# Kernel tuning notes

Measured on AMD Instinct MI355X. Metric: run time of the kernel, lower is better.

## Reference

```python
import jax, jax.numpy as jnp
import numpy as np

D_MODEL = 2048
HIDDEN = 1024
NUM_EXPERTS = 8
TOTAL_TOKENS = 16384  # tokens already sorted/grouped by expert


def setup_inputs() -> dict:
    key = jax.random.key(0)
    k1, k2, k3 = jax.random.split(key, 3)
    x = jax.random.normal(k1, (TOTAL_TOKENS, D_MODEL), dtype=jnp.float32)
    # nn.Linear(d_model, 2*E*H).weight -> [2*E*H, d_model]
    w_up_gate = jax.random.normal(k2, (2 * NUM_EXPERTS * HIDDEN, D_MODEL), dtype=jnp.float32) / np.sqrt(D_MODEL)
    # nn.Linear(E*H, d_model).weight -> [d_model, E*H]
    w_down = jax.random.normal(k3, (D_MODEL, NUM_EXPERTS * HIDDEN), dtype=jnp.float32) / np.sqrt(HIDDEN)
    batch_size_per_expert = jnp.full((NUM_EXPERTS,), TOTAL_TOKENS // NUM_EXPERTS, dtype=jnp.int32)
    return {
        "x": x,
        "w_up_gate": w_up_gate,
        "w_down": w_down,
        "batch_size_per_expert": batch_size_per_expert,
        "num_experts": NUM_EXPERTS,
    }


def reference(x, w_up_gate, w_down, batch_size_per_expert, num_experts):
    # Per-expert sizes are host constants (a Python list in the torch code).
    sizes = np.asarray(batch_size_per_expert)
    offs = np.concatenate([[0], np.cumsum(sizes)])  # static token offsets
    d_model = x.shape[-1]
    hidden = w_up_gate.shape[0] // (2 * num_experts)
    # [E, 2H, d_model]: expert e's fused up/gate weight block
    w_ug = w_up_gate.reshape(num_experts, 2 * hidden, d_model)
    outs = []
    for e in range(num_experts):  # small static loop over experts (ragged grouped GEMM)
        xe = x[offs[e]:offs[e + 1]]                      # [n_e, d_model]
        ug = xe @ w_ug[e].T                              # [n_e, 2H]
        h = jax.nn.silu(ug[:, :hidden]) * ug[:, hidden:]  # SwiGLU, [n_e, H]
        wd_e = w_down[:, e * hidden:(e + 1) * hidden]    # [d_model, H]
        outs.append(h @ wd_e.T)                          # [n_e, d_model]
    return jnp.concatenate(outs, axis=0)
```

## Files before the change

### kernel.cpp

```cpp
#include <hip/hip_runtime.h>
#include <hip/hip_bf16.h>

typedef __attribute__((ext_vector_type(8))) short short8;
typedef __attribute__((ext_vector_type(4))) float float4v;

#define BM 128
#define BK 32
#define LDSK 40

struct alignas(8) BF4 { unsigned short x, y, z, w; };
struct alignas(16) I4 { int x, y, z, w; };

__device__ __forceinline__ unsigned short f2bf(float f) {
    union { float f; unsigned u; } v; v.f = f;
    unsigned u = v.u + (0x7FFFu + ((v.u >> 16) & 1u));
    return (unsigned short)(u >> 16);
}

__device__ __forceinline__ void stage_f32_tile(const float* __restrict__ src, long ld,
                                               unsigned short* lds, int t) {
    const int rr  = t >> 3;
    const int col = (t & 7) << 2;
    #pragma unroll
    for (int r = 0; r < 4; ++r) {
        const int row = rr + r * 32;
        const float4 v = *(const float4*)(src + (long)row * ld + col);
        BF4 o; o.x = f2bf(v.x); o.y = f2bf(v.y); o.z = f2bf(v.z); o.w = f2bf(v.w);
        *(BF4*)(lds + row * LDSK + col) = o;
    }
}

__device__ __forceinline__ int find_expert(const int* __restrict__ bspe, int row0) {
    int e = 0, off = 0;
    #pragma unroll
    for (int i = 0; i < 8; ++i) {
        int s = bspe[i];
        if (row0 < off + s) { e = i; break; }
        off += s;
    }
    return e;
}

__global__ __launch_bounds__(256) void moe_up_gate(
    const float* __restrict__ x, const float* __restrict__ wug,
    const int* __restrict__ bspe, unsigned short* __restrict__ hws) {
    __shared__ alignas(16) unsigned short As[BM * LDSK];
    __shared__ alignas(16) unsigned short Bs[BM * LDSK];

    const int t = threadIdx.x;
    const int lane = t & 63;
    const int w = t >> 6;
    const int wr = w >> 1, wc = w & 1;
    const int bm = blockIdx.y;
    const int h0 = blockIdx.x * 64;
    const int row0 = bm * BM;

    const int e = find_expert(bspe, row0);

    const float* abase = x + (long)row0 * 2048;
    const float* bup = wug + ((long)e * 2048 + h0) * 2048;
    const float* bgt = wug + ((long)e * 2048 + 1024 + h0) * 2048;

    float4v acc[4][4];
    #pragma unroll
    for (int m = 0; m < 4; ++m)
        #pragma unroll
        for (int n = 0; n < 4; ++n)
            acc[m][n] = (float4v){0.f, 0.f, 0.f, 0.f};

    const int k8 = (lane >> 4) << 3;
    const int am = wr * 64 + (lane & 15);
    const int l15 = lane & 15;

    for (int k0 = 0; k0 < 2048; k0 += BK) {
        __syncthreads();
        stage_f32_tile(abase + k0, 2048, As, t);
        {
            const int rr  = t >> 3;
            const int col = (t & 7) << 2;
            #pragma unroll
            for (int r = 0; r < 4; ++r) {
                const int row = rr + r * 32;
                const float* p = (row < 64 ? bup + (long)row * 2048
                                           : bgt + (long)(row - 64) * 2048) + k0 + col;
                const float4 v = *(const float4*)p;
                BF4 o; o.x = f2bf(v.x); o.y = f2bf(v.y); o.z = f2bf(v.z); o.w = f2bf(v.w);
                *(BF4*)(Bs + row * LDSK + col) = o;
            }
        }
        __syncthreads();

        short8 a[4], b[4];
        #pragma unroll
        for (int m = 0; m < 4; ++m)
            a[m] = *(const short8*)(As + (am + m * 16) * LDSK + k8);
        #pragma unroll
        for (int n = 0; n < 4; ++n) {
            const int rb = (n < 2) ? (wc * 32 + n * 16) : (64 + wc * 32 + (n - 2) * 16);
            b[n] = *(const short8*)(Bs + (rb + l15) * LDSK + k8);
        }
        #pragma unroll
        for (int m = 0; m < 4; ++m)
            #pragma unroll
            for (int n = 0; n < 4; ++n)
                acc[m][n] = __builtin_amdgcn_mfma_f32_16x16x32_bf16(a[m], b[n], acc[m][n], 0, 0, 0);
    }

    const int rbase = row0 + wr * 64 + (lane >> 4) * 4;
    const int cbase = h0 + wc * 32 + l15;
    #pragma unroll
    for (int m = 0; m < 4; ++m)
        #pragma unroll
        for (int n = 0; n < 2; ++n)
            #pragma unroll
            for (int q = 0; q < 4; ++q) {
                const float u = acc[m][n][q];
                const float g = acc[m][n + 2][q];
                const float s = u / (1.f + __expf(-u));
                const int row = rbase + m * 16 + q;
                const int col = cbase + n * 16;
                hws[(long)row * 1024 + col] = f2bf(s * g);
            }
}

__global__ __launch_bounds__(256) void moe_down(
    const unsigned short* __restrict__ hws, const float* __restrict__ wd,
    const int* __restrict__ bspe, float* __restrict__ out) {
    __shared__ alignas(16) unsigned short As[BM * LDSK];
    __shared__ alignas(16) unsigned short Bs[BM * LDSK];

    const int t = threadIdx.x;
    const int lane = t & 63;
    const int w = t >> 6;
    const int wr = w >> 1, wc = w & 1;
    const int bm = blockIdx.y;
    const int n0 = blockIdx.x * BM;
    const int row0 = bm * BM;

    const int e = find_expert(bspe, row0);

    const unsigned short* abase = hws + (long)row0 * 1024;
    const float* bbase = wd + (long)n0 * 8192 + e * 1024;

    float4v acc[4][4];
    #pragma unroll
    for (int m = 0; m < 4; ++m)
        #pragma unroll
        for (int n = 0; n < 4; ++n)
            acc[m][n] = (float4v){0.f, 0.f, 0.f, 0.f};

    const int k8 = (lane >> 4) << 3;
    const int am = wr * 64 + (lane & 15);
    const int l15 = lane & 15;

    for (int k0 = 0; k0 < 1024; k0 += BK) {
        __syncthreads();
        {
            const int row = t >> 2;
            const int col = (t & 3) << 3;
            #pragma unroll
            for (int r = 0; r < 2; ++r) {
                const I4 v = *(const I4*)(abase + (long)(row + r * 64) * 1024 + k0 + col);
                *(I4*)(As + (row + r * 64) * LDSK + col) = v;
            }
        }
        stage_f32_tile(bbase + k0, 8192, Bs, t);
        __syncthreads();

        short8 a[4], b[4];
        #pragma unroll
        for (int m = 0; m < 4; ++m)
            a[m] = *(const short8*)(As + (am + m * 16) * LDSK + k8);
        #pragma unroll
        for (int n = 0; n < 4; ++n)
            b[n] = *(const short8*)(Bs + (wc * 64 + n * 16 + l15) * LDSK + k8);
        #pragma unroll
        for (int m = 0; m < 4; ++m)
            #pragma unroll
            for (int n = 0; n < 4; ++n)
                acc[m][n] = __builtin_amdgcn_mfma_f32_16x16x32_bf16(a[m], b[n], acc[m][n], 0, 0, 0);
    }

    const int rbase = row0 + wr * 64 + (lane >> 4) * 4;
    const int cbase = n0 + wc * 64 + l15;
    #pragma unroll
    for (int m = 0; m < 4; ++m)
        #pragma unroll
        for (int n = 0; n < 4; ++n)
            #pragma unroll
            for (int q = 0; q < 4; ++q)
                out[(long)(rbase + m * 16 + q) * 2048 + cbase + n * 16] = acc[m][n][q];
}

extern "C" void kernel_launch(void* const* d_in, const int* in_sizes, int n_in,
                              void* d_out, int out_size, void* d_ws, size_t ws_size,
                              hipStream_t stream) {
    const float* x   = (const float*)d_in[0];
    const float* wug = (const float*)d_in[1];
    const float* wd  = (const float*)d_in[2];
    const int*  bspe = (const int*)d_in[3];
    float* out = (float*)d_out;
    unsigned short* hws = (unsigned short*)d_ws;

    moe_up_gate<<<dim3(16, 128), dim3(256), 0, stream>>>(x, wug, bspe, hws);
    moe_down  <<<dim3(16, 128), dim3(256), 0, stream>>>(hws, wd, bspe, out);
}
```

Measured before the change: 680.8 us.

## Pre-convert inputs to bf16 and stage GEMM tiles via async global-to-LDS loads

Adds a single conversion kernel that casts x, the up/gate weights and the down weights to bf16 in workspace. Both grouped GEMMs then read bf16 directly and copy tiles into LDS with global_load_lds, replacing the per-tile fp32 load and convert in every block. This removes redundant re-conversion of the same tiles across blocks and halves the bytes read in the GEMM loops. In exchange it adds an extra pass over about 84M floats, needs a large workspace (otherwise the old fp32 path runs), and drops the LDS row padding, which may cause bank conflicts.

```diff
diff --git a/kernel.cpp b/kernel.cpp
--- a/kernel.cpp
+++ b/kernel.cpp
@@ -9,6 +9,7 @@
 #define LDSK 40
 
 struct alignas(8) BF4 { unsigned short x, y, z, w; };
+struct alignas(16) BF8 { BF4 a, b; };
 struct alignas(16) I4 { int x, y, z, w; };
 
 __device__ __forceinline__ unsigned short f2bf(float f) {
@@ -17,9 +18,188 @@
     return (unsigned short)(u >> 16);
 }
 
+__device__ __forceinline__ void async_copy16(const unsigned short* g, unsigned short* l) {
+    __builtin_amdgcn_global_load_lds(
+        (const __attribute__((address_space(1))) void*)g,
+        (__attribute__((address_space(3))) void*)l, 16, 0, 0);
+}
+
+__device__ __forceinline__ int find_expert(const int* __restrict__ bspe, int row0) {
+    int e = 0, off = 0;
+    #pragma unroll
+    for (int i = 0; i < 8; ++i) {
+        int s = bspe[i];
+        if (row0 < off + s) { e = i; break; }
+        off += s;
+    }
+    return e;
+}
+
+#define NX  33554432L
+#define NUG 33554432L
+#define NWD 16777216L
+
+__global__ void cvt_all(const float* __restrict__ x, const float* __restrict__ wug,
+                        const float* __restrict__ wd,
+                        unsigned short* __restrict__ xbf, unsigned short* __restrict__ wugbf,
+                        unsigned short* __restrict__ wdbf) {
+    const long TOT8 = (NX + NUG + NWD) / 8;
+    for (long i = (long)blockIdx.x * blockDim.x + threadIdx.x; i < TOT8;
+         i += (long)gridDim.x * blockDim.x) {
+        const long e0 = i * 8;
+        const float* s; unsigned short* d;
+        if (e0 < NX)            { s = x   + e0;              d = xbf   + e0; }
+        else if (e0 < NX + NUG) { s = wug + (e0 - NX);       d = wugbf + (e0 - NX); }
+        else                    { s = wd  + (e0 - NX - NUG); d = wdbf  + (e0 - NX - NUG); }
+        const float4 a = *(const float4*)s;
+        const float4 b = *(const float4*)(s + 4);
+        BF8 o;
+        o.a.x = f2bf(a.x); o.a.y = f2bf(a.y); o.a.z = f2bf(a.z); o.a.w = f2bf(a.w);
+        o.b.x = f2bf(b.x); o.b.y = f2bf(b.y); o.b.z = f2bf(b.z); o.b.w = f2bf(b.w);
+        *(BF8*)d = o;
+    }
+}
+
+__global__ __launch_bounds__(256) void moe_up_gate_v2(
+    const unsigned short* __restrict__ xbf, const unsigned short* __restrict__ wugbf,
+    const int* __restrict__ bspe, unsigned short* __restrict__ hbf) {
+    __shared__ alignas(16) unsigned short As[BM * BK];
+    __shared__ alignas(16) unsigned short Bs[BM * BK];
+
+    const int t = threadIdx.x, lane = t & 63, w = t >> 6;
+    const int wr = w >> 1, wc = w & 1;
+    const int h0 = blockIdx.x * 64, row0 = blockIdx.y * BM;
+    const int e = find_expert(bspe, row0);
+
+    const int srow = lane >> 2;
+    const int scol = (lane & 3) * 8;
+    const long aoff0 = (long)(row0 + w * 16 + srow) * 2048 + scol;
+    const long aoff1 = aoff0 + 64L * 2048;
+    const int brow = w * 16 + srow;
+    const long boff_up = ((long)e * 2048 + h0 + brow) * 2048 + scol;
+    const long boff_gt = ((long)e * 2048 + 1024 + h0 + brow) * 2048 + scol;
+    unsigned short* lA0 = As + w * 512;
+    unsigned short* lA1 = As + 2048 + w * 512;
+    unsigned short* lB0 = Bs + w * 512;
+    unsigned short* lB1 = Bs + 2048 + w * 512;
+
+    float4v acc[4][4];
+    #pragma unroll
+    for (int m = 0; m < 4; ++m)
+        #pragma unroll
+        for (int n = 0; n < 4; ++n) acc[m][n] = (float4v){0.f, 0.f, 0.f, 0.f};
+
+    const int k8 = (lane >> 4) << 3;
+    const int am = wr * 64 + (lane & 15);
+    const int l15 = lane & 15;
+
+    for (int k0 = 0; k0 < 2048; k0 += BK) {
+        __syncthreads();
+        async_copy16(xbf + aoff0 + k0, lA0);
+        async_copy16(xbf + aoff1 + k0, lA1);
+        async_copy16(wugbf + boff_up + k0, lB0);
+        async_copy16(wugbf + boff_gt + k0, lB1);
+        __syncthreads();
+
+        short8 a[4], b[4];
+        #pragma unroll
+        for (int m = 0; m < 4; ++m)
+            a[m] = *(const short8*)(As + (am + m * 16) * BK + k8);
+        #pragma unroll
+        for (int n = 0; n < 4; ++n) {
+            const int rb = (n < 2) ? (wc * 32 + n * 16) : (64 + wc * 32 + (n - 2) * 16);
+            b[n] = *(const short8*)(Bs + (rb + l15) * BK + k8);
+        }
+        #pragma unroll
+        for (int m = 0; m < 4; ++m)
+            #pragma unroll
+            for (int n = 0; n < 4; ++n)
+                acc[m][n] = __builtin_amdgcn_mfma_f32_16x16x32_bf16(a[m], b[n], acc[m][n], 0, 0, 0);
+    }
+
+    const int rbase = row0 + wr * 64 + (lane >> 4) * 4;
+    const int cbase = h0 + wc * 32 + l15;
+    #pragma unroll
+    for (int m = 0; m < 4; ++m)
+        #pragma unroll
+        for (int n = 0; n < 2; ++n)
+            #pragma unroll
+            for (int q = 0; q < 4; ++q) {
+                const float u = acc[m][n][q];
+                const float g = acc[m][n + 2][q];
+                const float s = u / (1.f + __expf(-u));
+                hbf[(long)(rbase + m * 16 + q) * 1024 + cbase + n * 16] = f2bf(s * g);
+            }
+}
+
+__global__ __launch_bounds__(256) void moe_down_v2(
+    const unsigned short* __restrict__ hbf, const unsigned short* __restrict__ wdbf,
+    const int* __restrict__ bspe, float* __restrict__ out) {
+    __shared__ alignas(16) unsigned short As[BM * BK];
+    __shared__ alignas(16) unsigned short Bs[BM * BK];
+
+    const int t = threadIdx.x, lane = t & 63, w = t >> 6;
+    const int wr = w >> 1, wc = w & 1;
+    const int n0 = blockIdx.x * BM, row0 = blockIdx.y * BM;
+    const int e = find_expert(bspe, row0);
+
+    const int srow = lane >> 2;
+    const int scol = (lane & 3) * 8;
+    const long aoff0 = (long)(row0 + w * 16 + srow) * 1024 + scol;
+    const long aoff1 = aoff0 + 64L * 1024;
+    const long boff0 = (long)(n0 + w * 16 + srow) * 8192 + e * 1024 + scol;
+    const long boff1 = boff0 + 64L * 8192;
+    unsigned short* lA0 = As + w * 512;
+    unsigned short* lA1 = As + 2048 + w * 512;
+    unsigned short* lB0 = Bs + w * 512;
+    unsigned short* lB1 = Bs + 2048 + w * 512;
+
+    float4v acc[4][4];
+    #pragma unroll
+    for (int m = 0; m < 4; ++m)
+        #pragma unroll
+        for (int n = 0; n < 4; ++n) acc[m][n] = (float4v){0.f, 0.f, 0.f, 0.f};
+
+    const int k8 = (lane >> 4) << 3;
+    const int am = wr * 64 + (lane & 15);
+    const int l15 = lane & 15;
+
+    for (int k0 = 0; k0 < 1024; k0 += BK) {
+        __syncthreads();
+        async_copy16(hbf + aoff0 + k0, lA0);
+        async_copy16(hbf + aoff1 + k0, lA1);
+        async_copy16(wdbf + boff0 + k0, lB0);
+        async_copy16(wdbf + boff1 + k0, lB1);
+        __syncthreads();
+
+        short8 a[4], b[4];
+        #pragma unroll
+        for (int m = 0; m < 4; ++m)
+            a[m] = *(const short8*)(As + (am + m * 16) * BK + k8);
+        #pragma unroll
+        for (int n = 0; n < 4; ++n)
+            b[n] = *(const short8*)(Bs + (wc * 64 + n * 16 + l15) * BK + k8);
+        #pragma unroll
+        for (int m = 0; m < 4; ++m)
+            #pragma unroll
+            for (int n = 0; n < 4; ++n)
+                acc[m][n] = __builtin_amdgcn_mfma_f32_16x16x32_bf16(a[m], b[n], acc[m][n], 0, 0, 0);
+    }
+
+    const int rbase = row0 + wr * 64 + (lane >> 4) * 4;
+    const int cbase = n0 + wc * 64 + l15;
+    #pragma unroll
+    for (int m = 0; m < 4; ++m)
+        #pragma unroll
+        for (int n = 0; n < 4; ++n)
+            #pragma unroll
+            for (int q = 0; q < 4; ++q)
+                out[(long)(rbase + m * 16 + q) * 2048 + cbase + n * 16] = acc[m][n][q];
+}
+
 __device__ __forceinline__ void stage_f32_tile(const float* __restrict__ src, long ld,
                                                unsigned short* lds, int t) {
-    const int rr  = t >> 3;
+    const int rr = t >> 3;
     const int col = (t & 7) << 2;
     #pragma unroll
     for (int r = 0; r < 4; ++r) {
@@ -30,54 +210,29 @@
     }
 }
 
-__device__ __forceinline__ int find_expert(const int* __restrict__ bspe, int row0) {
-    int e = 0, off = 0;
-    #pragma unroll
-    for (int i = 0; i < 8; ++i) {
-        int s = bspe[i];
-        if (row0 < off + s) { e = i; break; }
-        off += s;
-    }
-    return e;
-}
-
-__global__ __launch_bounds__(256) void moe_up_gate(
+__global__ __launch_bounds__(256) void moe_up_gate_fb(
     const float* __restrict__ x, const float* __restrict__ wug,
     const int* __restrict__ bspe, unsigned short* __restrict__ hws) {
     __shared__ alignas(16) unsigned short As[BM * LDSK];
     __shared__ alignas(16) unsigned short Bs[BM * LDSK];
-
-    const int t = threadIdx.x;
-    const int lane = t & 63;
-    const int w = t >> 6;
+    const int t = threadIdx.x, lane = t & 63, w = t >> 6;
     const int wr = w >> 1, wc = w & 1;
-    const int bm = blockIdx.y;
-    const int h0 = blockIdx.x * 64;
-    const int row0 = bm * BM;
-
+    const int h0 = blockIdx.x * 64, row0 = blockIdx.y * BM;
     const int e = find_expert(bspe, row0);
-
     const float* abase = x + (long)row0 * 2048;
     const float* bup = wug + ((long)e * 2048 + h0) * 2048;
     const float* bgt = wug + ((long)e * 2048 + 1024 + h0) * 2048;
-
     float4v acc[4][4];
     #pragma unroll
     for (int m = 0; m < 4; ++m)
         #pragma unroll
-        for (int n = 0; n < 4; ++n)
-            acc[m][n] = (float4v){0.f, 0.f, 0.f, 0.f};
-
-    const int k8 = (lane >> 4) << 3;
-    const int am = wr * 64 + (lane & 15);
-    const int l15 = lane & 15;
-
+        for (int n = 0; n < 4; ++n) acc[m][n] = (float4v){0.f, 0.f, 0.f, 0.f};
+    const int k8 = (lane >> 4) << 3, am = wr * 64 + (lane & 15), l15 = lane & 15;
     for (int k0 = 0; k0 < 2048; k0 += BK) {
         __syncthreads();
         stage_f32_tile(abase + k0, 2048, As, t);
         {
-            const int rr  = t >> 3;
-            const int col = (t & 7) << 2;
+            const int rr = t >> 3, col = (t & 7) << 2;
             #pragma unroll
             for (int r = 0; r < 4; ++r) {
                 const int row = rr + r * 32;
@@ -89,11 +244,9 @@
             }
         }
         __syncthreads();
-
         short8 a[4], b[4];
         #pragma unroll
-        for (int m = 0; m < 4; ++m)
-            a[m] = *(const short8*)(As + (am + m * 16) * LDSK + k8);
+        for (int m = 0; m < 4; ++m) a[m] = *(const short8*)(As + (am + m * 16) * LDSK + k8);
         #pragma unroll
         for (int n = 0; n < 4; ++n) {
             const int rb = (n < 2) ? (wc * 32 + n * 16) : (64 + wc * 32 + (n - 2) * 16);
@@ -105,7 +258,6 @@
             for (int n = 0; n < 4; ++n)
                 acc[m][n] = __builtin_amdgcn_mfma_f32_16x16x32_bf16(a[m], b[n], acc[m][n], 0, 0, 0);
     }
-
     const int rbase = row0 + wr * 64 + (lane >> 4) * 4;
     const int cbase = h0 + wc * 32 + l15;
     #pragma unroll
@@ -114,50 +266,33 @@
         for (int n = 0; n < 2; ++n)
             #pragma unroll
             for (int q = 0; q < 4; ++q) {
-                const float u = acc[m][n][q];
-                const float g = acc[m][n + 2][q];
+                const float u = acc[m][n][q], g = acc[m][n + 2][q];
                 const float s = u / (1.f + __expf(-u));
-                const int row = rbase + m * 16 + q;
-                const int col = cbase + n * 16;
-                hws[(long)row * 1024 + col] = f2bf(s * g);
+                hws[(long)(rbase + m * 16 + q) * 1024 + cbase + n * 16] = f2bf(s * g);
             }
 }
 
-__global__ __launch_bounds__(256) void moe_down(
+__global__ __launch_bounds__(256) void moe_down_fb(
     const unsigned short* __restrict__ hws, const float* __restrict__ wd,
     const int* __restrict__ bspe, float* __restrict__ out) {
     __shared__ alignas(16) unsigned short As[BM * LDSK];
     __shared__ alignas(16) unsigned short Bs[BM * LDSK];
-
-    const int t = threadIdx.x;
-    const int lane = t & 63;
-    const int w = t >> 6;
+    const int t = threadIdx.x, lane = t & 63, w = t >> 6;
     const int wr = w >> 1, wc = w & 1;
-    const int bm = blockIdx.y;
-    const int n0 = blockIdx.x * BM;
-    const int row0 = bm * BM;
-
+    const int n0 = blockIdx.x * BM, row0 = blockIdx.y * BM;
     const int e = find_expert(bspe, row0);
-
     const unsigned short* abase = hws + (long)row0 * 1024;
     const float* bbase = wd + (long)n0 * 8192 + e * 1024;
-
     float4v acc[4][4];
     #pragma unroll
     for (int m = 0; m < 4; ++m)
         #pragma unroll
-        for (int n = 0; n < 4; ++n)
-            acc[m][n] = (float4v){0.f, 0.f, 0.f, 0.f};
-
-    const int k8 = (lane >> 4) << 3;
-    const int am = wr * 64 + (lane & 15);
-    const int l15 = lane & 15;
-
+        for (int n = 0; n < 4; ++n) acc[m][n] = (float4v){0.f, 0.f, 0.f, 0.f};
+    const int k8 = (lane >> 4) << 3, am = wr * 64 + (lane & 15), l15 = lane & 15;
     for (int k0 = 0; k0 < 1024; k0 += BK) {
         __syncthreads();
         {
-            const int row = t >> 2;
-            const int col = (t & 3) << 3;
+            const int row = t >> 2, col = (t & 3) << 3;
             #pragma unroll
             for (int r = 0; r < 2; ++r) {
                 const I4 v = *(const I4*)(abase + (long)(row + r * 64) * 1024 + k0 + col);
@@ -166,21 +301,17 @@
         }
         stage_f32_tile(bbase + k0, 8192, Bs, t);
         __syncthreads();
-
         short8 a[4], b[4];
         #pragma unroll
-        for (int m = 0; m < 4; ++m)
-            a[m] = *(const short8*)(As + (am + m * 16) * LDSK + k8);
-        #pragma unroll
-        for (int n = 0; n < 4; ++n)
-            b[n] = *(const short8*)(Bs + (wc * 64 + n * 16 + l15) * LDSK + k8);
+        for (int m = 0; m < 4; ++m) a[m] = *(const short8*)(As + (am + m * 16) * LDSK + k8);
+        #pragma unroll
+        for (int n = 0; n < 4; ++n) b[n] = *(const short8*)(Bs + (wc * 64 + n * 16 + l15) * LDSK + k8);
         #pragma unroll
         for (int m = 0; m < 4; ++m)
             #pragma unroll
             for (int n = 0; n < 4; ++n)
                 acc[m][n] = __builtin_amdgcn_mfma_f32_16x16x32_bf16(a[m], b[n], acc[m][n], 0, 0, 0);
     }
-
     const int rbase = row0 + wr * 64 + (lane >> 4) * 4;
     const int cbase = n0 + wc * 64 + l15;
     #pragma unroll
@@ -200,8 +331,19 @@
     const float* wd  = (const float*)d_in[2];
     const int*  bspe = (const int*)d_in[3];
     float* out = (float*)d_out;
-    unsigned short* hws = (unsigned short*)d_ws;
-
-    moe_up_gate<<<dim3(16, 128), dim3(256), 0, stream>>>(x, wug, bspe, hws);
-    moe_down  <<<dim3(16, 128), dim3(256), 0, stream>>>(hws, wd, bspe, out);
-}
+
+    const size_t need = (size_t)(NX + NUG + NWD + 16777216L) * 2;
+    if (ws_size >= need) {
+        unsigned short* xbf   = (unsigned short*)d_ws;
+        unsigned short* wugbf = xbf + NX;
+        unsigned short* wdbf  = wugbf + NUG;
+        unsigned short* hbf   = wdbf + NWD;
+        cvt_all<<<dim3(8192), dim3(256), 0, stream>>>(x, wug, wd, xbf, wugbf, wdbf);
+        moe_up_gate_v2<<<dim3(16, 128), dim3(256), 0, stream>>>(xbf, wugbf, bspe, hbf);
+        moe_down_v2  <<<dim3(16, 128), dim3(256), 0, stream>>>(hbf, wdbf, bspe, out);
+    } else {
+        unsigned short* hws = (unsigned short*)d_ws;
+        moe_up_gate_fb<<<dim3(16, 128), dim3(256), 0, stream>>>(x, wug, bspe, hws);
+        moe_down_fb  <<<dim3(16, 128), dim3(256), 0, stream>>>(hws, wd, bspe, out);
+    }
+}
```

Measured after the change: 694.2 us. Within noise of the previous version (+2.0%).
